# Kernel optimization log

Measured on AMD Instinct MI355X. Metric: run time of the kernel, lower is better.

Reference implementation:

```python
import jax, jax.numpy as jnp
import numpy as np

N, E, F_IN, HID, HEADS, CLASSES = 50000, 800000, 128, 128, 4, 2
NEG_SLOPE = 0.2


def _gatv2_layer(x, Wl, Wr, att, bias, src, dst, heads, concat):
    # PyG GATv2Conv (share_weights=False, eval mode):
    #   e_ij = att . leaky_relu(Wl x_j + Wr x_i); alpha = segment_softmax over dst;
    #   out_i = sum_j alpha_ij * (Wl x_j)
    n = x.shape[0]
    c = att.shape[-1]
    xl = (x @ Wl).reshape(n, heads, c)   # source transform [N,H,C]
    xr = (x @ Wr).reshape(n, heads, c)   # target transform [N,H,C]
    e = jax.nn.leaky_relu(xl[src] + xr[dst], NEG_SLOPE)      # [E,H,C]
    logits = jnp.einsum('ehc,hc->eh', e, att)                # [E,H]
    m = jax.ops.segment_max(logits, dst, num_segments=n)     # stable softmax per dst
    p = jnp.exp(logits - m[dst])
    denom = jax.ops.segment_sum(p, dst, num_segments=n)
    alpha = p / (denom[dst] + 1e-16)                         # [E,H]
    out = jax.ops.segment_sum(alpha[:, :, None] * xl[src], dst, num_segments=n)  # [N,H,C]
    out = out.reshape(n, heads * c) if concat else out.mean(axis=1)
    return out + bias


def setup_inputs() -> dict:
    key = jax.random.key(0)
    ks = jax.random.split(key, 16)
    s = lambda fan_in: 1.0 / np.sqrt(fan_in)
    inp = {
        'x': jax.random.normal(ks[0], (N, F_IN), jnp.float32),
        'edge_idx': jax.random.randint(ks[1], (2, E), 0, N, jnp.int64),
        'w_in': jax.random.normal(ks[2], (F_IN, HID), jnp.float32) * s(F_IN),
        'b_in': jnp.zeros((HID,), jnp.float32),
        'wl1': jax.random.normal(ks[3], (HID, HEADS * HID), jnp.float32) * s(HID),
        'wr1': jax.random.normal(ks[4], (HID, HEADS * HID), jnp.float32) * s(HID),
        'att1': jax.random.normal(ks[5], (HEADS, HID), jnp.float32) * s(HID),
        'b1': jnp.zeros((HEADS * HID,), jnp.float32),
        'wl2': jax.random.normal(ks[6], (HEADS * HID, HID), jnp.float32) * s(HEADS * HID),
        'wr2': jax.random.normal(ks[7], (HEADS * HID, HID), jnp.float32) * s(HEADS * HID),
        'att2': jax.random.normal(ks[8], (1, HID), jnp.float32) * s(HID),
        'b2': jnp.zeros((HID,), jnp.float32),
        'w_out': jax.random.normal(ks[9], (HID, CLASSES), jnp.float32) * s(HID),
        'b_out': jnp.zeros((CLASSES,), jnp.float32),
    }
    return inp


def reference(x, edge_idx, w_in, b_in, wl1, wr1, att1, b1, wl2, wr2, att2, b2, w_out, b_out):
    n = x.shape[0]
    loops = jnp.arange(n, dtype=edge_idx.dtype)  # PyG add_self_loops=True
    src = jnp.concatenate([edge_idx[0], loops])
    dst = jnp.concatenate([edge_idx[1], loops])
    h = jax.nn.elu(x @ w_in + b_in)              # dropout is identity in eval
    h = jax.nn.elu(_gatv2_layer(h, wl1, wr1, att1, b1, src, dst, HEADS, True))
    h = jax.nn.elu(_gatv2_layer(h, wl2, wr2, att2, b2, src, dst, 1, False))
    logits = h @ w_out + b_out
    return jax.nn.log_softmax(logits, axis=1)
```

## Files before the change

### kernel.cpp

```cpp
#include <hip/hip_runtime.h>
#include <hip/hip_bf16.h>
#include <math.h>

#define F_IN   128
#define HID    128
#define HEADS  4
#define HC1    (HEADS*HID)
#define CLASSES 2
#define NEG_SLOPE 0.2f
#define LOG2E 1.44269504088896340736f
#define MNEG  -3.0e38f

#define SCAN_CHUNK 2048

typedef __attribute__((ext_vector_type(8))) short short8;
typedef __attribute__((ext_vector_type(4))) float f32x4;
typedef __attribute__((ext_vector_type(2))) float f32x2;

__device__ __forceinline__ f32x2 unpack2(unsigned u) {
    f32x2 r;
    r.x = __uint_as_float(u << 16);
    r.y = __uint_as_float(u & 0xffff0000u);
    return r;
}

__global__ void zero_int_kernel(int* __restrict__ p, int n) {
    int i = blockIdx.x * blockDim.x + threadIdx.x;
    int stride = gridDim.x * blockDim.x;
    for (; i < n; i += stride) p[i] = 0;
}

__global__ void deg_kernel(const int* __restrict__ dst_arr, int* __restrict__ deg,
                           int E, int N) {
    int e = blockIdx.x * blockDim.x + threadIdx.x;
    if (e >= E) return;
    int d = dst_arr[e];
    if ((unsigned)d >= (unsigned)N) d = 0;
    atomicAdd(&deg[d], 1);
}

__global__ void scan_partial_kernel(const int* __restrict__ deg, int* __restrict__ bsum, int n) {
    __shared__ int sdata[256];
    int b = blockIdx.x, t = threadIdx.x;
    int base = b * SCAN_CHUNK;
    int s = 0;
    for (int i = t; i < SCAN_CHUNK; i += 256) {
        int idx = base + i;
        s += (idx < n) ? deg[idx] : 0;
    }
    sdata[t] = s;
    __syncthreads();
    for (int off = 128; off; off >>= 1) {
        if (t < off) sdata[t] += sdata[t + off];
        __syncthreads();
    }
    if (t == 0) bsum[b] = sdata[0];
}

__global__ void scan_bsums_kernel(int* __restrict__ bsum, int nb, int* __restrict__ row, int n) {
    if (blockIdx.x == 0 && threadIdx.x == 0) {
        int acc = 0;
        for (int i = 0; i < nb; ++i) { int v = bsum[i]; bsum[i] = acc; acc += v; }
        row[n] = acc;
    }
}

__global__ void scan_final_kernel(const int* __restrict__ deg, const int* __restrict__ bsum,
                                  int* __restrict__ row, int* __restrict__ cursor, int n) {
    __shared__ int tsum[256];
    int b = blockIdx.x, t = threadIdx.x;
    int base = b * SCAN_CHUNK + t * 8;
    int local[8];
    int s = 0;
    #pragma unroll
    for (int k = 0; k < 8; ++k) {
        int idx = base + k;
        int v = (idx < n) ? deg[idx] : 0;
        local[k] = s;
        s += v;
    }
    tsum[t] = s;
    __syncthreads();
    for (int off = 1; off < 256; off <<= 1) {
        int v = 0;
        if (t >= off) v = tsum[t - off];
        __syncthreads();
        if (t >= off) tsum[t] += v;
        __syncthreads();
    }
    int texcl = (t == 0) ? 0 : tsum[t - 1];
    int boff = bsum[b];
    #pragma unroll
    for (int k = 0; k < 8; ++k) {
        int idx = base + k;
        if (idx < n) {
            int v = boff + texcl + local[k];
            row[idx] = v;
            cursor[idx] = v;
        }
    }
}

__global__ void scatter_kernel(const int* __restrict__ src_arr, const int* __restrict__ dst_arr,
                               int* __restrict__ cursor, int* __restrict__ src_sorted,
                               int E, int N) {
    int e = blockIdx.x * blockDim.x + threadIdx.x;
    if (e >= E) return;
    int s = src_arr[e], d = dst_arr[e];
    if ((unsigned)s >= (unsigned)N) s = 0;
    if ((unsigned)d >= (unsigned)N) d = 0;
    int pos = atomicAdd(&cursor[d], 1);
    src_sorted[pos] = s;
}

__global__ void weights_prep_kernel(
    const float* __restrict__ w_in, const float* __restrict__ wl1,
    const float* __restrict__ wr1, const float* __restrict__ wl2,
    const float* __restrict__ wr2,
    __hip_bfloat16* __restrict__ w_inT, __hip_bfloat16* __restrict__ wT1,
    __hip_bfloat16* __restrict__ wT2)
{
    int t = blockIdx.x * blockDim.x + threadIdx.x;
    const int S0 = 128 * 128, S1 = 128 * 512;
    if (t < S0) {
        int n = t / 128, k = t % 128;
        w_inT[t] = __float2bfloat16(w_in[(size_t)k * 128 + n]);
    } else if (t < S0 + S1) {
        int idx = t - S0;
        int n = idx / 128, k = idx % 128;
        wT1[idx] = __float2bfloat16(wl1[(size_t)k * 512 + n]);
    } else if (t < S0 + 2 * S1) {
        int idx = t - S0 - S1;
        int n = idx / 128, k = idx % 128;
        wT1[(size_t)(512 + n) * 128 + k] = __float2bfloat16(wr1[(size_t)k * 512 + n]);
    } else if (t < S0 + 3 * S1) {
        int idx = t - S0 - 2 * S1;
        int n = idx / 512, k = idx % 512;
        wT2[idx] = __float2bfloat16(wl2[(size_t)k * 128 + n]);
    } else if (t < S0 + 4 * S1) {
        int idx = t - S0 - 3 * S1;
        int n = idx / 512, k = idx % 512;
        wT2[(size_t)(128 + n) * 512 + k] = __float2bfloat16(wr2[(size_t)k * 128 + n]);
    }
}

template<int ACT, typename AT, typename OutT>
__global__ __launch_bounds__(256) void mfma_gemm_kernel(
    const AT* __restrict__ A,
    const __hip_bfloat16* __restrict__ BT,
    const float* __restrict__ bias,
    OutT* __restrict__ C,
    int M, int K, int N)
{
    constexpr int BM = 128, BN = 128, BK = 64, LDA = 72;
    __shared__ __align__(16) short As[BM * LDA];
    __shared__ __align__(16) short Bs[BN * LDA];

    const int tid  = threadIdx.x;
    const int lane = tid & 63;
    const int wid  = tid >> 6;
    const int wm   = wid >> 1;
    const int wn   = wid & 1;
    const int fr   = lane & 15;
    const int fk   = (lane >> 4) * 8;

    const int row0 = blockIdx.y * BM;
    const int col0 = blockIdx.x * BN;

    const short* Bg = (const short*)BT;

    f32x4 acc[4][4] = {};

    for (int k0 = 0; k0 < K; k0 += BK) {
        #pragma unroll
        for (int it = 0; it < 4; ++it) {
            int chunk = it * 256 + tid;
            int r = chunk >> 3, c = chunk & 7;
            int gr = row0 + r;
            short8 v = {0, 0, 0, 0, 0, 0, 0, 0};
            if (gr < M) {
                if constexpr (sizeof(AT) == 2) {
                    v = *(const short8*)((const short*)A + (size_t)gr * K + k0 + c * 8);
                } else {
                    const float* ap = (const float*)A + (size_t)gr * K + k0 + c * 8;
                    float4 a0 = *(const float4*)ap;
                    float4 a1 = *(const float4*)(ap + 4);
                    __hip_bfloat16 h;
                    h = __float2bfloat16(a0.x); v[0] = *(short*)&h;
                    h = __float2bfloat16(a0.y); v[1] = *(short*)&h;
                    h = __float2bfloat16(a0.z); v[2] = *(short*)&h;
                    h = __float2bfloat16(a0.w); v[3] = *(short*)&h;
                    h = __float2bfloat16(a1.x); v[4] = *(short*)&h;
                    h = __float2bfloat16(a1.y); v[5] = *(short*)&h;
                    h = __float2bfloat16(a1.z); v[6] = *(short*)&h;
                    h = __float2bfloat16(a1.w); v[7] = *(short*)&h;
                }
            }
            *(short8*)(&As[r * LDA + c * 8]) = v;
        }
        #pragma unroll
        for (int it = 0; it < 4; ++it) {
            int chunk = it * 256 + tid;
            int n = chunk >> 3, c = chunk & 7;
            short8 v = *(const short8*)(Bg + (size_t)(col0 + n) * K + k0 + c * 8);
            *(short8*)(&Bs[n * LDA + c * 8]) = v;
        }
        __syncthreads();
        #pragma unroll
        for (int kk = 0; kk < 2; ++kk) {
            short8 af[4], bf[4];
            #pragma unroll
            for (int i = 0; i < 4; ++i)
                af[i] = *(const short8*)(&As[(wm * 64 + i * 16 + fr) * LDA + kk * 32 + fk]);
            #pragma unroll
            for (int j = 0; j < 4; ++j)
                bf[j] = *(const short8*)(&Bs[(wn * 64 + j * 16 + fr) * LDA + kk * 32 + fk]);
            #pragma unroll
            for (int i = 0; i < 4; ++i)
                #pragma unroll
                for (int j = 0; j < 4; ++j)
                    acc[i][j] = __builtin_amdgcn_mfma_f32_16x16x32_bf16(af[i], bf[j], acc[i][j], 0, 0, 0);
        }
        __syncthreads();
    }

    const int crow = row0 + wm * 64;
    const int ccol = col0 + wn * 64;
    #pragma unroll
    for (int i = 0; i < 4; ++i) {
        #pragma unroll
        for (int j = 0; j < 4; ++j) {
            int col = ccol + j * 16 + (lane & 15);
            float bv = bias ? bias[col] : 0.0f;
            #pragma unroll
            for (int reg = 0; reg < 4; ++reg) {
                int r = crow + i * 16 + (lane >> 4) * 4 + reg;
                if (r < M) {
                    float v = acc[i][j][reg] + bv;
                    if (ACT == 1) v = (v > 0.0f) ? v : expm1f(v);
                    C[(size_t)r * N + col] = (OutT)v;
                }
            }
        }
    }
}

__global__ __launch_bounds__(256) void gatv2_l1_fused_kernel(
    const __hip_bfloat16* __restrict__ xlr,
    const int* __restrict__ row, const int* __restrict__ src_sorted,
    const float* __restrict__ att, const float* __restrict__ b1,
    __hip_bfloat16* __restrict__ out1, int N)
{
    int d = blockIdx.x * 4 + (threadIdx.x >> 6);
    if (d >= N) return;
    int lane = threadIdx.x & 63;
    int cbase = lane * 8;
    const short* basep = (const short*)xlr;

    f32x2 xrd2[4], attv2[4];
    {
        uint4 raw = *reinterpret_cast<const uint4*>(basep + (size_t)d * 1024 + 512 + cbase);
        const unsigned* u = reinterpret_cast<const unsigned*>(&raw);
        #pragma unroll
        for (int j = 0; j < 4; ++j) xrd2[j] = unpack2(u[j]);
        #pragma unroll
        for (int j = 0; j < 4; ++j) {
            attv2[j].x = att[cbase + 2 * j] * LOG2E;
            attv2[j].y = att[cbase + 2 * j + 1] * LOG2E;
        }
    }

    float m = MNEG;
    float s = 0.0f;
    f32x2 o2[4] = {};

    int rs = row[d], re = row[d + 1];

    uint4 raw = *reinterpret_cast<const uint4*>(basep + (size_t)d * 1024 + cbase);
    for (int it = rs - 1; it < re; ++it) {
        uint4 cur = raw;
        if (it + 1 < re) {
            int sn = src_sorted[it + 1];
            raw = *reinterpret_cast<const uint4*>(basep + (size_t)sn * 1024 + cbase);
        }
        const unsigned* u = reinterpret_cast<const unsigned*>(&cur);
        f32x2 v2[4];
        #pragma unroll
        for (int j = 0; j < 4; ++j) v2[j] = unpack2(u[j]);

        f32x2 tacc = {0.0f, 0.0f};
        #pragma unroll
        for (int j = 0; j < 4; ++j) {
            f32x2 e = v2[j] + xrd2[j];
            f32x2 ne = e * NEG_SLOPE;
            e.x = fmaxf(e.x, ne.x);
            e.y = fmaxf(e.y, ne.y);
            tacc = __builtin_elementwise_fma(e, attv2[j], tacc);
        }
        float t = tacc.x + tacc.y;
        t += __shfl_xor(t, 1);
        t += __shfl_xor(t, 2);
        t += __shfl_xor(t, 4);
        t += __shfl_xor(t, 8);
        if (t > m) {
            float r = exp2f(m - t);
            s *= r;
            f32x2 r2 = {r, r};
            #pragma unroll
            for (int j = 0; j < 4; ++j) o2[j] *= r2;
            m = t;
        }
        float p = exp2f(t - m);
        s += p;
        f32x2 p2 = {p, p};
        #pragma unroll
        for (int j = 0; j < 4; ++j) o2[j] = __builtin_elementwise_fma(p2, v2[j], o2[j]);
    }

    float inv = 1.0f / (s + 1e-16f);
    short8 sv;
    #pragma unroll
    for (int j = 0; j < 4; ++j) {
        #pragma unroll
        for (int h = 0; h < 2; ++h) {
            float val = ((h == 0) ? o2[j].x : o2[j].y) * inv + b1[cbase + 2 * j + h];
            val = (val > 0.0f) ? val : expm1f(val);
            __hip_bfloat16 hb = __float2bfloat16(val);
            sv[2 * j + h] = *reinterpret_cast<short*>(&hb);
        }
    }
    *(short8*)((short*)out1 + (size_t)d * HC1 + cbase) = sv;
}

__global__ __launch_bounds__(256) void gatv2_l2_final_kernel(
    const __hip_bfloat16* __restrict__ xlr2,
    const int* __restrict__ row, const int* __restrict__ src_sorted,
    const float* __restrict__ att2, const float* __restrict__ b2,
    const float* __restrict__ w_out, const float* __restrict__ b_out,
    float* __restrict__ out, int N)
{
    int d = blockIdx.x * 4 + (threadIdx.x >> 6);
    if (d >= N) return;
    int lane = threadIdx.x & 63;
    int g  = lane >> 4;
    int gl = lane & 15;
    int cbase = gl * 8;
    const short* basep = (const short*)xlr2;

    f32x2 xrd2[4], attv2[4];
    {
        uint4 rawx = *reinterpret_cast<const uint4*>(basep + (size_t)d * 256 + 128 + cbase);
        const unsigned* u = reinterpret_cast<const unsigned*>(&rawx);
        #pragma unroll
        for (int j = 0; j < 4; ++j) xrd2[j] = unpack2(u[j]);
        #pragma unroll
        for (int j = 0; j < 4; ++j) {
            attv2[j].x = att2[cbase + 2 * j] * LOG2E;
            attv2[j].y = att2[cbase + 2 * j + 1] * LOG2E;
        }
    }

    float m = MNEG;
    float s = 0.0f;
    f32x2 o2[4] = {};

    int rs = row[d], re = row[d + 1];
    int L = re - rs + 1;

    for (int p0 = g; p0 < L; p0 += 4) {
        int srcn = (p0 == 0) ? d : src_sorted[rs + p0 - 1];
        uint4 cur = *reinterpret_cast<const uint4*>(basep + (size_t)srcn * 256 + cbase);
        const unsigned* u = reinterpret_cast<const unsigned*>(&cur);
        f32x2 v2[4];
        #pragma unroll
        for (int j = 0; j < 4; ++j) v2[j] = unpack2(u[j]);

        f32x2 tacc = {0.0f, 0.0f};
        #pragma unroll
        for (int j = 0; j < 4; ++j) {
            f32x2 e = v2[j] + xrd2[j];
            f32x2 ne = e * NEG_SLOPE;
            e.x = fmaxf(e.x, ne.x);
            e.y = fmaxf(e.y, ne.y);
            tacc = __builtin_elementwise_fma(e, attv2[j], tacc);
        }
        float t = tacc.x + tacc.y;
        t += __shfl_xor(t, 1);
        t += __shfl_xor(t, 2);
        t += __shfl_xor(t, 4);
        t += __shfl_xor(t, 8);
        if (t > m) {
            float r = exp2f(m - t);
            s *= r;
            f32x2 r2 = {r, r};
            #pragma unroll
            for (int j = 0; j < 4; ++j) o2[j] *= r2;
            m = t;
        }
        float p = exp2f(t - m);
        s += p;
        f32x2 p2 = {p, p};
        #pragma unroll
        for (int j = 0; j < 4; ++j) o2[j] = __builtin_elementwise_fma(p2, v2[j], o2[j]);
    }

    #pragma unroll
    for (int off = 16; off <= 32; off <<= 1) {
        float m_o = __shfl_xor(m, off);
        float s_o = __shfl_xor(s, off);
        f32x2 oo[4];
        #pragma unroll
        for (int j = 0; j < 4; ++j) {
            oo[j].x = __shfl_xor(o2[j].x, off);
            oo[j].y = __shfl_xor(o2[j].y, off);
        }
        float mn = fmaxf(m, m_o);
        float a = exp2f(m - mn);
        float b = exp2f(m_o - mn);
        s = s * a + s_o * b;
        f32x2 a2 = {a, a}, b2v = {b, b};
        #pragma unroll
        for (int j = 0; j < 4; ++j)
            o2[j] = o2[j] * a2 + oo[j] * b2v;
        m = mn;
    }

    float inv = 1.0f / (s + 1e-16f);
    float a0 = 0.0f, a1 = 0.0f;
    #pragma unroll
    for (int j = 0; j < 4; ++j) {
        #pragma unroll
        for (int h = 0; h < 2; ++h) {
            int c = cbase + 2 * j + h;
            float val = ((h == 0) ? o2[j].x : o2[j].y) * inv + b2[c];
            val = (val > 0.0f) ? val : expm1f(val);
            a0 = fmaf(val, w_out[c * 2 + 0], a0);
            a1 = fmaf(val, w_out[c * 2 + 1], a1);
        }
    }
    #pragma unroll
    for (int off = 1; off <= 8; off <<= 1) {
        a0 += __shfl_xor(a0, off);
        a1 += __shfl_xor(a1, off);
    }
    if (lane == 0) {
        float z0 = a0 + b_out[0];
        float z1 = a1 + b_out[1];
        float mx = fmaxf(z0, z1);
        float lse = mx + logf(__expf(z0 - mx) + __expf(z1 - mx));
        out[(size_t)d * CLASSES + 0] = z0 - lse;
        out[(size_t)d * CLASSES + 1] = z1 - lse;
    }
}

extern "C" void kernel_launch(void* const* d_in, const int* in_sizes, int n_in,
                              void* d_out, int out_size, void* d_ws, size_t ws_size,
                              hipStream_t stream)
{
    const float* x     = (const float*)d_in[0];
    const int*   eidx  = (const int*)d_in[1];
    const float* w_in  = (const float*)d_in[2];
    const float* b_in  = (const float*)d_in[3];
    const float* wl1   = (const float*)d_in[4];
    const float* wr1   = (const float*)d_in[5];
    const float* att1  = (const float*)d_in[6];
    const float* b1    = (const float*)d_in[7];
    const float* wl2   = (const float*)d_in[8];
    const float* wr2   = (const float*)d_in[9];
    const float* att2  = (const float*)d_in[10];
    const float* b2    = (const float*)d_in[11];
    const float* w_out = (const float*)d_in[12];
    const float* b_out = (const float*)d_in[13];
    float* out = (float*)d_out;

    const int N = in_sizes[0] / F_IN;
    const int E = in_sizes[1] / 2;
    const int* src_arr = eidx;
    const int* dst_arr = eidx + E;

    size_t off = 0;
    auto alloc = [&](size_t bytes) -> char* {
        char* ptr = (char*)d_ws + off;
        off += (bytes + 255) & ~(size_t)255;
        return ptr;
    };
    int* row        = (int*)alloc((size_t)(N + 1) * 4);
    int* cursor     = (int*)alloc((size_t)N * 4);
    int* deg        = (int*)alloc((size_t)N * 4);
    int* bsum       = (int*)alloc(64 * 4);
    int* src_sorted = (int*)alloc((size_t)E * 4);
    __hip_bfloat16* w_inT = (__hip_bfloat16*)alloc((size_t)F_IN * HID * 2);
    __hip_bfloat16* wT1   = (__hip_bfloat16*)alloc((size_t)2 * HC1 * HID * 2);
    __hip_bfloat16* wT2   = (__hip_bfloat16*)alloc((size_t)2 * HID * HC1 * 2);
    __hip_bfloat16* h0b   = (__hip_bfloat16*)alloc((size_t)N * HID * 2);
    __hip_bfloat16* xlr1  = (__hip_bfloat16*)alloc((size_t)N * 2 * HC1 * 2);
    __hip_bfloat16* out1  = (__hip_bfloat16*)alloc((size_t)N * HC1 * 2);

    __hip_bfloat16* xlr2 = xlr1;

    dim3 blk(256);
    const int NB_SCAN = (N + SCAN_CHUNK - 1) / SCAN_CHUNK;

    hipLaunchKernelGGL(zero_int_kernel, dim3(64), blk, 0, stream, deg, N);
    hipLaunchKernelGGL(deg_kernel, dim3((E + 255) / 256), blk, 0, stream, dst_arr, deg, E, N);
    hipLaunchKernelGGL(scan_partial_kernel, dim3(NB_SCAN), blk, 0, stream, deg, bsum, N);
    hipLaunchKernelGGL(scan_bsums_kernel, dim3(1), blk, 0, stream, bsum, NB_SCAN, row, N);
    hipLaunchKernelGGL(scan_final_kernel, dim3(NB_SCAN), blk, 0, stream, deg, bsum, row, cursor, N);
    hipLaunchKernelGGL(scatter_kernel, dim3((E + 255) / 256), blk, 0, stream,
                       src_arr, dst_arr, cursor, src_sorted, E, N);

    {
        int total = 128 * 128 + 4 * 128 * 512;
        hipLaunchKernelGGL(weights_prep_kernel, dim3((total + 255) / 256), blk, 0, stream,
                           w_in, wl1, wr1, wl2, wr2, w_inT, wT1, wT2);
    }
    {
        dim3 grid(HID / 128, (N + 127) / 128);
        hipLaunchKernelGGL((mfma_gemm_kernel<1, float, __hip_bfloat16>), grid, blk, 0, stream,
                           x, w_inT, b_in, h0b, N, F_IN, HID);
    }
    {
        dim3 grid(2 * HC1 / 128, (N + 127) / 128);
        hipLaunchKernelGGL((mfma_gemm_kernel<0, __hip_bfloat16, __hip_bfloat16>), grid, blk, 0, stream,
                           h0b, wT1, (const float*)nullptr, xlr1, N, HID, 2 * HC1);
    }
    {
        dim3 grid((N + 3) / 4);
        hipLaunchKernelGGL(gatv2_l1_fused_kernel, grid, blk, 0, stream,
                           xlr1, row, src_sorted, att1, b1, out1, N);
    }
    {
        dim3 grid(2 * HID / 128, (N + 127) / 128);
        hipLaunchKernelGGL((mfma_gemm_kernel<0, __hip_bfloat16, __hip_bfloat16>), grid, blk, 0, stream,
                           out1, wT2, (const float*)nullptr, xlr2, N, HC1, 2 * HID);
    }
    {
        dim3 grid((N + 3) / 4);
        hipLaunchKernelGGL(gatv2_l2_final_kernel, grid, blk, 0, stream,
                           xlr2, row, src_sorted, att2, b2, w_out, b_out, out, N);
    }
}
```

Measured before the change: 578.5 us.

## Fuse input projection GEMM with layer-1 Wl/Wr GEMM via shared-memory hidden tile

Merges the input linear+ELU GEMM and the layer-1 source/target projection GEMM into one kernel. Each block computes a 128-row tile of h0 in shared memory as bf16, then reuses it as the A operand for four 128-column output tiles. This removes the h0 round trip through global memory and one launch. The cost is that the first GEMM is recomputed by both column blocks (grid x=2), and the larger shared-memory footprint may lower occupancy.

```diff
diff --git a/kernel.cpp b/kernel.cpp
--- a/kernel.cpp
+++ b/kernel.cpp
@@ -144,17 +144,15 @@
     }
 }
 
-template<int ACT, typename AT, typename OutT>
-__global__ __launch_bounds__(256) void mfma_gemm_kernel(
-    const AT* __restrict__ A,
-    const __hip_bfloat16* __restrict__ BT,
-    const float* __restrict__ bias,
-    OutT* __restrict__ C,
-    int M, int K, int N)
+__global__ __launch_bounds__(256) void l1_merged_kernel(
+    const float* __restrict__ x, const __hip_bfloat16* __restrict__ w_inT,
+    const float* __restrict__ b_in, const __hip_bfloat16* __restrict__ wT1,
+    __hip_bfloat16* __restrict__ xlr1, int M)
 {
-    constexpr int BM = 128, BN = 128, BK = 64, LDA = 72;
-    __shared__ __align__(16) short As[BM * LDA];
-    __shared__ __align__(16) short Bs[BN * LDA];
+    constexpr int LDA = 136, LDB = 72;
+    __shared__ __align__(16) short As[128 * LDA];
+    __shared__ __align__(16) short Bs[128 * LDB];
+    short* Ws = As;
 
     const int tid  = threadIdx.x;
     const int lane = tid & 63;
@@ -163,26 +161,20 @@
     const int wn   = wid & 1;
     const int fr   = lane & 15;
     const int fk   = (lane >> 4) * 8;
-
-    const int row0 = blockIdx.y * BM;
-    const int col0 = blockIdx.x * BN;
-
-    const short* Bg = (const short*)BT;
-
-    f32x4 acc[4][4] = {};
-
-    for (int k0 = 0; k0 < K; k0 += BK) {
-        #pragma unroll
-        for (int it = 0; it < 4; ++it) {
-            int chunk = it * 256 + tid;
-            int r = chunk >> 3, c = chunk & 7;
-            int gr = row0 + r;
-            short8 v = {0, 0, 0, 0, 0, 0, 0, 0};
-            if (gr < M) {
-                if constexpr (sizeof(AT) == 2) {
-                    v = *(const short8*)((const short*)A + (size_t)gr * K + k0 + c * 8);
-                } else {
-                    const float* ap = (const float*)A + (size_t)gr * K + k0 + c * 8;
+    const int row0 = blockIdx.y * 128;
+
+    {
+        f32x4 acc[4][4] = {};
+        for (int k0 = 0; k0 < 128; k0 += 64) {
+            __syncthreads();
+            #pragma unroll
+            for (int it = 0; it < 4; ++it) {
+                int chunk = it * 256 + tid;
+                int r = chunk >> 3, c = chunk & 7;
+                int gr = row0 + r;
+                short8 v = {0, 0, 0, 0, 0, 0, 0, 0};
+                if (gr < M) {
+                    const float* ap = x + (size_t)gr * 128 + k0 + c * 8;
                     float4 a0 = *(const float4*)ap;
                     float4 a1 = *(const float4*)(ap + 4);
                     __hip_bfloat16 h;
@@ -195,7 +187,135 @@
                     h = __float2bfloat16(a1.z); v[6] = *(short*)&h;
                     h = __float2bfloat16(a1.w); v[7] = *(short*)&h;
                 }
-            }
+                *(short8*)(&Bs[r * LDB + c * 8]) = v;
+            }
+            #pragma unroll
+            for (int it = 0; it < 4; ++it) {
+                int chunk = it * 256 + tid;
+                int n = chunk >> 3, c = chunk & 7;
+                short8 v = *(const short8*)((const short*)w_inT + (size_t)n * 128 + k0 + c * 8);
+                *(short8*)(&Ws[n * LDB + c * 8]) = v;
+            }
+            __syncthreads();
+            #pragma unroll
+            for (int kk = 0; kk < 2; ++kk) {
+                short8 af[4], bf[4];
+                #pragma unroll
+                for (int i = 0; i < 4; ++i)
+                    af[i] = *(const short8*)(&Bs[(wm * 64 + i * 16 + fr) * LDB + kk * 32 + fk]);
+                #pragma unroll
+                for (int j = 0; j < 4; ++j)
+                    bf[j] = *(const short8*)(&Ws[(wn * 64 + j * 16 + fr) * LDB + kk * 32 + fk]);
+                #pragma unroll
+                for (int i = 0; i < 4; ++i)
+                    #pragma unroll
+                    for (int j = 0; j < 4; ++j)
+                        acc[i][j] = __builtin_amdgcn_mfma_f32_16x16x32_bf16(af[i], bf[j], acc[i][j], 0, 0, 0);
+            }
+        }
+        __syncthreads();
+        #pragma unroll
+        for (int i = 0; i < 4; ++i) {
+            #pragma unroll
+            for (int j = 0; j < 4; ++j) {
+                int col = wn * 64 + j * 16 + fr;
+                float bv = b_in[col];
+                #pragma unroll
+                for (int reg = 0; reg < 4; ++reg) {
+                    int r = wm * 64 + i * 16 + (lane >> 4) * 4 + reg;
+                    float v = acc[i][j][reg] + bv;
+                    v = (v > 0.0f) ? v : expm1f(v);
+                    __hip_bfloat16 hb = __float2bfloat16(v);
+                    As[r * LDA + col] = *reinterpret_cast<short*>(&hb);
+                }
+            }
+        }
+        __syncthreads();
+    }
+
+    const int colBase = blockIdx.x * 4;
+    for (int ct = 0; ct < 4; ++ct) {
+        const int col0 = (colBase + ct) * 128;
+        f32x4 acc[4][4] = {};
+        for (int k0 = 0; k0 < 128; k0 += 64) {
+            __syncthreads();
+            #pragma unroll
+            for (int it = 0; it < 4; ++it) {
+                int chunk = it * 256 + tid;
+                int n = chunk >> 3, c = chunk & 7;
+                short8 v = *(const short8*)((const short*)wT1 + (size_t)(col0 + n) * 128 + k0 + c * 8);
+                *(short8*)(&Bs[n * LDB + c * 8]) = v;
+            }
+            __syncthreads();
+            #pragma unroll
+            for (int kk = 0; kk < 2; ++kk) {
+                short8 af[4], bf[4];
+                #pragma unroll
+                for (int i = 0; i < 4; ++i)
+                    af[i] = *(const short8*)(&As[(wm * 64 + i * 16 + fr) * LDA + k0 + kk * 32 + fk]);
+                #pragma unroll
+                for (int j = 0; j < 4; ++j)
+                    bf[j] = *(const short8*)(&Bs[(wn * 64 + j * 16 + fr) * LDB + kk * 32 + fk]);
+                #pragma unroll
+                for (int i = 0; i < 4; ++i)
+                    #pragma unroll
+                    for (int j = 0; j < 4; ++j)
+                        acc[i][j] = __builtin_amdgcn_mfma_f32_16x16x32_bf16(af[i], bf[j], acc[i][j], 0, 0, 0);
+            }
+        }
+        const int crow = row0 + wm * 64;
+        const int ccol = col0 + wn * 64;
+        #pragma unroll
+        for (int i = 0; i < 4; ++i) {
+            #pragma unroll
+            for (int j = 0; j < 4; ++j) {
+                int col = ccol + j * 16 + fr;
+                #pragma unroll
+                for (int reg = 0; reg < 4; ++reg) {
+                    int r = crow + i * 16 + (lane >> 4) * 4 + reg;
+                    if (r < M) xlr1[(size_t)r * 1024 + col] = (__hip_bfloat16)acc[i][j][reg];
+                }
+            }
+        }
+    }
+}
+
+template<int ACT, typename OutT>
+__global__ __launch_bounds__(256) void mfma_gemm_kernel(
+    const __hip_bfloat16* __restrict__ A,
+    const __hip_bfloat16* __restrict__ BT,
+    const float* __restrict__ bias,
+    OutT* __restrict__ C,
+    int M, int K, int N)
+{
+    constexpr int LDA = 72;
+    __shared__ __align__(16) short As[128 * LDA];
+    __shared__ __align__(16) short Bs[128 * LDA];
+
+    const int tid  = threadIdx.x;
+    const int lane = tid & 63;
+    const int wid  = tid >> 6;
+    const int wm   = wid >> 1;
+    const int wn   = wid & 1;
+    const int fr   = lane & 15;
+    const int fk   = (lane >> 4) * 8;
+
+    const int row0 = blockIdx.y * 128;
+    const int col0 = blockIdx.x * 128;
+
+    const short* Ag = (const short*)A;
+    const short* Bg = (const short*)BT;
+
+    f32x4 acc[4][4] = {};
+
+    for (int k0 = 0; k0 < K; k0 += 64) {
+        #pragma unroll
+        for (int it = 0; it < 4; ++it) {
+            int chunk = it * 256 + tid;
+            int r = chunk >> 3, c = chunk & 7;
+            int gr = row0 + r;
+            short8 v = {0, 0, 0, 0, 0, 0, 0, 0};
+            if (gr < M) v = *(const short8*)(Ag + (size_t)gr * K + k0 + c * 8);
             *(short8*)(&As[r * LDA + c * 8]) = v;
         }
         #pragma unroll
@@ -492,7 +612,6 @@
     __hip_bfloat16* w_inT = (__hip_bfloat16*)alloc((size_t)F_IN * HID * 2);
     __hip_bfloat16* wT1   = (__hip_bfloat16*)alloc((size_t)2 * HC1 * HID * 2);
     __hip_bfloat16* wT2   = (__hip_bfloat16*)alloc((size_t)2 * HID * HC1 * 2);
-    __hip_bfloat16* h0b   = (__hip_bfloat16*)alloc((size_t)N * HID * 2);
     __hip_bfloat16* xlr1  = (__hip_bfloat16*)alloc((size_t)N * 2 * HC1 * 2);
     __hip_bfloat16* out1  = (__hip_bfloat16*)alloc((size_t)N * HC1 * 2);
 
@@ -500,6 +619,7 @@
 
     dim3 blk(256);
     const int NB_SCAN = (N + SCAN_CHUNK - 1) / SCAN_CHUNK;
+    const int nRowBlk = (N + 127) / 128;
 
     hipLaunchKernelGGL(zero_int_kernel, dim3(64), blk, 0, stream, deg, N);
     hipLaunchKernelGGL(deg_kernel, dim3((E + 255) / 256), blk, 0, stream, dst_arr, deg, E, N);
@@ -515,28 +635,17 @@
                            w_in, wl1, wr1, wl2, wr2, w_inT, wT1, wT2);
     }
     {
-        dim3 grid(HID / 128, (N + 127) / 128);
-        hipLaunchKernelGGL((mfma_gemm_kernel<1, float, __hip_bfloat16>), grid, blk, 0, stream,
-                           x, w_inT, b_in, h0b, N, F_IN, HID);
-    }
+        dim3 grid(2, nRowBlk);
+        hipLaunchKernelGGL(l1_merged_kernel, grid, blk, 0, stream,
+                           x, w_inT, b_in, wT1, xlr1, N);
+    }
+    hipLaunchKernelGGL(gatv2_l1_fused_kernel, dim3((N + 3) / 4), blk, 0, stream,
+                       xlr1, row, src_sorted, att1, b1, out1, N);
     {
-        dim3 grid(2 * HC1 / 128, (N + 127) / 128);
-        hipLaunchKernelGGL((mfma_gemm_kernel<0, __hip_bfloat16, __hip_bfloat16>), grid, blk, 0, stream,
-                           h0b, wT1, (const float*)nullptr, xlr1, N, HID, 2 * HC1);
-    }
-    {
-        dim3 grid((N + 3) / 4);
-        hipLaunchKernelGGL(gatv2_l1_fused_kernel, grid, blk, 0, stream,
-                           xlr1, row, src_sorted, att1, b1, out1, N);
-    }
-    {
-        dim3 grid(2 * HID / 128, (N + 127) / 128);
-        hipLaunchKernelGGL((mfma_gemm_kernel<0, __hip_bfloat16, __hip_bfloat16>), grid, blk, 0, stream,
+        dim3 grid(2 * HID / 128, nRowBlk);
+        hipLaunchKernelGGL((mfma_gemm_kernel<0, __hip_bfloat16>), grid, blk, 0, stream,
                            out1, wT2, (const float*)nullptr, xlr2, N, HC1, 2 * HID);
     }
-    {
-        dim3 grid((N + 3) / 4);
-        hipLaunchKernelGGL(gatv2_l2_final_kernel, grid, blk, 0, stream,
-                           xlr2, row, src_sorted, att2, b2, w_out, b_out, out, N);
-    }
-}
+    hipLaunchKernelGGL(gatv2_l2_final_kernel, dim3((N + 3) / 4), blk, 0, stream,
+                       xlr2, row, src_sorted, att2, b2, w_out, b_out, out, N);
+}
```

New measurement: 551.1 us. 1.05x faster.
